# Performance work log

Hardware: AMD Instinct MI355X
Metric: run time of the kernel (lower is better)

The kernel has to match this reference:

```python
import jax, jax.numpy as jnp
import numpy as np

B, L, D = 2, 2048, 1024
H = 16          # num_heads
HD = D // H     # head_dim = 64
NEG_INF = jnp.float32(-1e30)


def setup_inputs() -> dict:
    key = jax.random.key(0)
    ks = jax.random.split(key, 10)
    s = 1.0 / np.sqrt(D)
    return {
        "x": jax.random.normal(ks[0], (B, L, D), dtype=jnp.float32),
        "Wq": jax.random.normal(ks[1], (D, D), dtype=jnp.float32) * s,
        "bq": jnp.zeros((D,), jnp.float32),
        "Wk": jax.random.normal(ks[2], (D, D), dtype=jnp.float32) * s,
        "bk": jnp.zeros((D,), jnp.float32),
        "Wv": jax.random.normal(ks[3], (D, D), dtype=jnp.float32) * s,
        "bv": jnp.zeros((D,), jnp.float32),
        "Wo": jax.random.normal(ks[4], (D, D), dtype=jnp.float32) * s,
        "bo": jnp.zeros((D,), jnp.float32),
        "local_scale": jnp.ones((1,), jnp.float32),
        "global_scale": jnp.ones((1,), jnp.float32),
    }


def reference(x, Wq, bq, Wk, bk, Wv, bv, Wo, bo, local_scale, global_scale):
    # projections -> [B, H, L, HD]
    def proj(W, b):
        return (x @ W + b).reshape(B, L, H, HD).transpose(0, 2, 1, 3)
    Q, K, V = proj(Wq, bq), proj(Wk, bk), proj(Wv, bv)
    lh = H // 2
    inv_sqrt = 1.0 / jnp.sqrt(jnp.float32(HD))

    # local (causal) heads
    scores_l = jnp.einsum("bhqd,bhkd->bhqk", Q[:, :lh], K[:, :lh]) * inv_sqrt
    causal = jnp.tril(jnp.ones((L, L), dtype=bool))  # keep lower triangle
    scores_l = jnp.where(causal, scores_l * local_scale, NEG_INF)
    attn_local = jax.nn.softmax(scores_l, axis=-1)
    out_local = jnp.einsum("bhqk,bhkd->bhqd", attn_local, V[:, :lh])

    # global (full) heads
    scores_g = jnp.einsum("bhqd,bhkd->bhqk", Q[:, lh:], K[:, lh:]) * inv_sqrt
    attn_global = jax.nn.softmax(scores_g * global_scale, axis=-1)
    out_global = jnp.einsum("bhqk,bhkd->bhqd", attn_global, V[:, lh:])

    out = jnp.concatenate([out_local, out_global], axis=1)  # [B,H,L,HD]
    out = out.transpose(0, 2, 1, 3).reshape(B, L, D)
    out = out @ Wo + bo
    return (out, attn_local, attn_global)
```

## Files before the change

### kernel.cpp

```cpp
#include <hip/hip_runtime.h>
#include <hip/hip_bf16.h>

#define B 2
#define L 2048
#define D 1024
#define H 16
#define HD 64
#define LH 8
#define NEG_INF -1e30f

typedef __hip_bfloat16 bf16;
typedef unsigned short ushort_t;
typedef short bf16x8 __attribute__((ext_vector_type(8)));
typedef unsigned short us8 __attribute__((ext_vector_type(8)));
typedef float f32x4 __attribute__((ext_vector_type(4)));

#define MFMA16(a, b, c) __builtin_amdgcn_mfma_f32_16x16x32_bf16((a), (b), (c), 0, 0, 0)

#define WAITBAR(N) do {                                              \
    asm volatile("s_waitcnt vmcnt(" #N ") lgkmcnt(0)" ::: "memory"); \
    __builtin_amdgcn_sched_barrier(0);                               \
    __builtin_amdgcn_s_barrier();                                    \
  } while (0)

#define LGKM0_FENCE() do {                                  \
    asm volatile("s_waitcnt lgkmcnt(0)" ::: "memory");      \
    __builtin_amdgcn_sched_barrier(0);                      \
  } while (0)

#if defined(__has_builtin)
#if __has_builtin(__builtin_amdgcn_global_load_lds)
#define HAVE_GLOAD_LDS 1
#endif
#endif

template<typename T> struct IsF32;
template<> struct IsF32<float> { static constexpr int value = 1; };
template<> struct IsF32<bf16>  { static constexpr int value = 0; };

__device__ __forceinline__ float ldf(const float* p, size_t i) { return p[i]; }
__device__ __forceinline__ float ldf(const bf16* p, size_t i) { return __bfloat162float(p[i]); }

__device__ __forceinline__ float4 ld4(const float* p, size_t i) {
  return *reinterpret_cast<const float4*>(p + i);
}
__device__ __forceinline__ float4 ld4(const bf16* p, size_t i) {
  ushort4 u = *reinterpret_cast<const ushort4*>(p + i);
  float4 f;
  f.x = __uint_as_float(((unsigned)u.x) << 16);
  f.y = __uint_as_float(((unsigned)u.y) << 16);
  f.z = __uint_as_float(((unsigned)u.z) << 16);
  f.w = __uint_as_float(((unsigned)u.w) << 16);
  return f;
}
__device__ __forceinline__ ushort_t bfh(float v) {
  bf16 h = __float2bfloat16(v);
  return *reinterpret_cast<ushort_t*>(&h);
}
__device__ __forceinline__ float bf2f(ushort_t u) {
  return __uint_as_float(((unsigned)u) << 16);
}
__device__ __forceinline__ void stf(float* p, size_t i, float v) { p[i] = v; }
__device__ __forceinline__ void stf(bf16* p, size_t i, float v) { p[i] = __float2bfloat16(v); }

__device__ __forceinline__ int swz(int row, int slot) {
  return row * 64 + (((slot ^ (row & 7)) & 7) << 3);
}
__device__ __forceinline__ int swzc(int row, int c) {
  return row * 64 + (((((c >> 3) ^ row) & 7) << 3) | (c & 7));
}

#if defined(HAVE_GLOAD_LDS)
__device__ __forceinline__ void gload_lds16(const ushort_t* src, ushort_t* dst) {
  __builtin_amdgcn_global_load_lds(
      (const __attribute__((address_space(1))) unsigned int*)src,
      (__attribute__((address_space(3))) unsigned int*)dst, 16, 0, 0);
}
#endif

__device__ __forceinline__ void stage64(const ushort_t* g, size_t gstride,
                                        ushort_t* lds, int w, int ln) {
  #pragma unroll
  for (int c = 0; c < 2; ++c) {
    const int row = 16 * w + 8 * c + (ln >> 3);
    const int slot = ((ln & 7) ^ row) & 7;
    const ushort_t* src = g + (size_t)row * gstride + slot * 8;
#if defined(HAVE_GLOAD_LDS)
    gload_lds16(src, lds + (size_t)(16 * w + 8 * c) * 64);
#else
    *reinterpret_cast<uint4*>(&lds[row * 64 + (ln & 7) * 8]) =
        *reinterpret_cast<const uint4*>(src);
#endif
  }
}

__global__ void detect_dtype_kernel(const unsigned short* __restrict__ x,
                                    int* __restrict__ flag) {
  int bad = 0;
  for (int i = threadIdx.x; i < 1024; i += 64) {
    if (((x[i] >> 7) & 0xFF) >= 170) bad = 1;
  }
  unsigned long long m = __ballot(bad);
  if (threadIdx.x == 0) *flag = (m != 0ULL) ? 1 : 0;
}

__global__ __launch_bounds__(256)
void cast_f32_kernel(const int* __restrict__ flag, int want,
                     const float* __restrict__ in,
                     ushort_t* __restrict__ hp, int n4) {
  if (*flag != want) return;
  int i = blockIdx.x * 256 + threadIdx.x;
  const int stride = gridDim.x * 256;
  for (; i < n4; i += stride) {
    float4 v = *reinterpret_cast<const float4*>(in + 4 * (size_t)i);
    ushort4 h;
    h.x = bfh(v.x); h.y = bfh(v.y); h.z = bfh(v.z); h.w = bfh(v.w);
    *reinterpret_cast<ushort4*>(hp + 4 * (size_t)i) = h;
  }
}

template<typename T>
__global__ __launch_bounds__(256)
void transW_kernel(const int* __restrict__ flag,
                   const T* __restrict__ W0, const T* __restrict__ W1,
                   const T* __restrict__ W2, const T* __restrict__ W3,
                   ushort_t* __restrict__ base, ushort_t* __restrict__ baseWo) {
  if (*flag != IsF32<T>::value) return;
  const int z = blockIdx.z;
  const T* W = z == 0 ? W0 : (z == 1 ? W1 : (z == 2 ? W2 : W3));
  ushort_t* hp = (z < 3) ? (base + (size_t)z * 2097152) : baseWo;
  __shared__ float ts[64][69];
  const int k0 = blockIdx.x * 64, n0 = blockIdx.y * 64;
  const int t = threadIdx.x;
  #pragma unroll
  for (int p = 0; p < 4; ++p) {
    int r = p * 16 + (t >> 4);
    int c = (t & 15) * 4;
    float4 v = ld4(W, (size_t)(k0 + r) * D + n0 + c);
    ts[r][c] = v.x; ts[r][c + 1] = v.y; ts[r][c + 2] = v.z; ts[r][c + 3] = v.w;
  }
  __syncthreads();
  #pragma unroll
  for (int p = 0; p < 4; ++p) {
    int n = p * 16 + (t >> 4);
    int k4 = (t & 15) * 4;
    ushort4 h;
    h.x = bfh(ts[k4][n]);
    h.y = bfh(ts[k4 + 1][n]);
    h.z = bfh(ts[k4 + 2][n]);
    h.w = bfh(ts[k4 + 3][n]);
    *reinterpret_cast<ushort4*>(&hp[(size_t)(n0 + n) * D + k0 + k4]) = h;
  }
}

template<typename T>
__global__ __launch_bounds__(256, 5)
void gemm_kernel(const int* __restrict__ flag,
                 const ushort_t* __restrict__ xA, const ushort_t* __restrict__ aoh,
                 const ushort_t* __restrict__ wbase, const ushort_t* __restrict__ woT,
                 const T* __restrict__ bq, const T* __restrict__ bk,
                 const T* __restrict__ bv, const T* __restrict__ bo,
                 ushort_t* __restrict__ qh, ushort_t* __restrict__ kh,
                 ushort_t* __restrict__ vth, T* __restrict__ out0, int zfix) {
  if (*flag != IsF32<T>::value) return;
  const int cpx = gridDim.x >> 3;
  const int swzid = ((int)blockIdx.x & 7) * cpx + ((int)blockIdx.x >> 3);
  const int mtile = swzid & 63;
  const int ntile = (swzid >> 6) & 15;
  const int z = (zfix >= 0) ? zfix : (swzid >> 10);
  const int m0 = mtile * 64, n0 = ntile * 64;

  const bool isOut = (z == 3);
  const ushort_t* Ah = isOut ? aoh : xA;
  const ushort_t* wh = isOut ? woT : (wbase + (size_t)z * 2097152);

  __shared__ ushort_t As[2][4096], Bs[2][4096];

  const int ln = threadIdx.x & 63, w = threadIdx.x >> 6;
  const int m = ln & 15, hi = ln >> 4;

  f32x4 acc[4] = {};

  stage64(Ah + (size_t)m0 * 1024, 1024, As[0], w, ln);
  stage64(wh + (size_t)n0 * 1024, 1024, Bs[0], w, ln);
  __syncthreads();
  for (int step = 0; step < 16; ++step) {
    const int cur = step & 1;
    if (step < 15) {
      stage64(Ah + (size_t)m0 * 1024 + (step + 1) * 64, 1024, As[cur ^ 1], w, ln);
      stage64(wh + (size_t)n0 * 1024 + (step + 1) * 64, 1024, Bs[cur ^ 1], w, ln);
    }
    __builtin_amdgcn_s_setprio(1);
    #pragma unroll
    for (int kc = 0; kc < 2; ++kc) {
      bf16x8 a_h = *reinterpret_cast<const bf16x8*>(&As[cur][swz(16 * w + m, kc * 4 + hi)]);
      bf16x8 b_h[4];
      #pragma unroll
      for (int f = 0; f < 4; ++f)
        b_h[f] = *reinterpret_cast<const bf16x8*>(&Bs[cur][swz(f * 16 + m, kc * 4 + hi)]);
      #pragma unroll
      for (int fc = 0; fc < 4; ++fc)
        acc[fc] = MFMA16(a_h, b_h[fc], acc[fc]);
    }
    __builtin_amdgcn_s_setprio(0);
    __syncthreads();
  }

  #pragma unroll
  for (int fc = 0; fc < 4; ++fc) {
    const int col = n0 + fc * 16 + m;
    if (isOut) {
      const float bv_ = ldf(bo, (size_t)col);
      #pragma unroll
      for (int r = 0; r < 4; ++r) {
        const int tok = m0 + 16 * w + 4 * hi + r;
        stf(out0, (size_t)tok * D + col, acc[fc][r] + bv_);
      }
    } else if (z == 2) {
      const int hh = col >> 6, d = col & 63;
      const float bv_ = ldf(bv, (size_t)col);
      const int tok0 = m0 + 16 * w + 4 * hi;
      const int bb = tok0 >> 11, ll = tok0 & (L - 1);
      ushort4 hv;
      hv.x = bfh(acc[fc][0] + bv_);
      hv.y = bfh(acc[fc][1] + bv_);
      hv.z = bfh(acc[fc][2] + bv_);
      hv.w = bfh(acc[fc][3] + bv_);
      *reinterpret_cast<ushort4*>(
          &vth[((size_t)(bb * H + hh) * HD + d) * L + ll]) = hv;
    } else {
      const int hh = col >> 6, d = col & 63;
      const float bv_ = ldf(z == 0 ? bq : bk, (size_t)col);
      ushort_t* oh = z == 0 ? qh : kh;
      #pragma unroll
      for (int r = 0; r < 4; ++r) {
        const int tok = m0 + 16 * w + 4 * hi + r;
        const int bb = tok >> 11, ll = tok & (L - 1);
        oh[((size_t)(bb * H + hh) * L + ll) * HD + d] = bfh(acc[fc][r] + bv_);
      }
    }
  }
}

template<typename T>
__global__ __launch_bounds__(256, 4)
void attn_kernel(const int* __restrict__ flag,
                 const ushort_t* __restrict__ Qh_g, const ushort_t* __restrict__ Kh_g,
                 const ushort_t* __restrict__ Vth_g,
                 const T* __restrict__ lsp, const T* __restrict__ gsp,
                 T* __restrict__ attn_l, T* __restrict__ attn_g,
                 ushort_t* __restrict__ AOh) {
  if (*flag != IsF32<T>::value) return;
  const int bid = blockIdx.x;
  const int xcd = bid & 7, slot = bid >> 3;
  const int bhg = xcd + 8 * (slot >> 5);
  const int strip_raw = slot & 31;
  const int bb = bhg >> 4, h = bhg & 15;
  const bool is_local = h < LH;
  const int strip = is_local ? (31 - strip_raw) : strip_raw;
  const int q0 = strip * 64;
  const int ln = threadIdx.x & 63, w = threadIdx.x >> 6;
  const int m = ln & 15, hi = ln >> 4;

  const float cscale =
      (is_local ? ldf(lsp, (size_t)0) : ldf(gsp, (size_t)0)) * 0.125f;
  const size_t bh_off = ((size_t)bb * H + h) * L * HD;
  const ushort_t* Qhb = Qh_g + bh_off;
  const ushort_t* Khb = Kh_g + bh_off;
  const ushort_t* Vhb = Vth_g + bh_off;

  __shared__ ushort_t SH[20480];
  ushort_t* Ps = SH + 16384;

  bf16x8 qfh[2];
  {
    const size_t qb = (size_t)(q0 + 16 * w + m) * HD + hi * 8;
    qfh[0] = *reinterpret_cast<const bf16x8*>(Qhb + qb);
    qfh[1] = *reinterpret_cast<const bf16x8*>(Qhb + qb + 32);
  }

  float m_ = NEG_INF, l_ = 0.f;
  const int nkt = is_local ? (strip + 1) : (L / 64);
  T* aout = is_local ? attn_l : attn_g;
  const size_t arow0 =
      ((size_t)(bb * LH + (is_local ? h : h - LH)) * L + q0) * L;

  stage64(Khb, HD, SH, w, ln);
  WAITBAR(0);
  for (int kt = 0; kt < nkt; ++kt) {
    const int cur = kt & 1;
    if (kt + 1 < nkt)
      stage64(Khb + (size_t)((kt + 1) * 64) * HD, HD, SH + (cur ^ 1) * 4096, w, ln);

    const ushort_t* Kc = SH + cur * 4096;
    f32x4 s[4] = {};
    __builtin_amdgcn_s_setprio(1);
    #pragma unroll
    for (int nt = 0; nt < 4; ++nt)
      #pragma unroll
      for (int kc = 0; kc < 2; ++kc) {
        bf16x8 kbh = *reinterpret_cast<const bf16x8*>(&Kc[swz(nt * 16 + m, kc * 4 + hi)]);
        s[nt] = MFMA16(kbh, qfh[kc], s[nt]);
      }
    __builtin_amdgcn_s_setprio(0);

    const bool dg = is_local && (kt == strip);
    #pragma unroll
    for (int nt = 0; nt < 4; ++nt)
      #pragma unroll
      for (int r = 0; r < 4; ++r) {
        float v = s[nt][r] * cscale;
        if (dg && (nt * 16 + 4 * hi + r > 16 * w + m)) v = NEG_INF;
        s[nt][r] = v;
      }
    float tm = NEG_INF;
    #pragma unroll
    for (int nt = 0; nt < 4; ++nt)
      #pragma unroll
      for (int r = 0; r < 4; ++r) tm = fmaxf(tm, s[nt][r]);
    tm = fmaxf(tm, __shfl_xor(tm, 16, 64));
    tm = fmaxf(tm, __shfl_xor(tm, 32, 64));
    const float mn = fmaxf(m_, tm);
    float sum = 0.f;
    #pragma unroll
    for (int nt = 0; nt < 4; ++nt)
      #pragma unroll
      for (int r = 0; r < 4; ++r) sum += __expf(s[nt][r] - mn);
    sum += __shfl_xor(sum, 16, 64);
    sum += __shfl_xor(sum, 32, 64);
    l_ = l_ * __expf(m_ - mn) + sum;
    m_ = mn;
    WAITBAR(0);
  }

  const float invl = 1.0f / l_;
  f32x4 o_[4] = {};

  stage64(Khb, HD, SH, w, ln);
  stage64(Vhb, L, SH + 8192, w, ln);
  WAITBAR(0);
  for (int kt = 0; kt < nkt; ++kt) {
    const int cur = kt & 1;
    if (kt + 1 < nkt) {
      stage64(Khb + (size_t)((kt + 1) * 64) * HD, HD, SH + (cur ^ 1) * 4096, w, ln);
      stage64(Vhb + (size_t)((kt + 1) * 64), L, SH + 8192 + (cur ^ 1) * 4096, w, ln);
    }
    const ushort_t* Kc = SH + cur * 4096;
    const ushort_t* Vc = SH + 8192 + cur * 4096;

    f32x4 s[4] = {};
    __builtin_amdgcn_s_setprio(1);
    #pragma unroll
    for (int nt = 0; nt < 4; ++nt)
      #pragma unroll
      for (int kc = 0; kc < 2; ++kc) {
        bf16x8 kbh = *reinterpret_cast<const bf16x8*>(&Kc[swz(nt * 16 + m, kc * 4 + hi)]);
        s[nt] = MFMA16(kbh, qfh[kc], s[nt]);
      }
    __builtin_amdgcn_s_setprio(0);

    const bool dg = is_local && (kt == strip);
    #pragma unroll
    for (int nt = 0; nt < 4; ++nt) {
      float v0 = s[nt][0] * cscale, v1 = s[nt][1] * cscale;
      float v2 = s[nt][2] * cscale, v3 = s[nt][3] * cscale;
      if (dg) {
        const int kbq = nt * 16 + 4 * hi, qq = 16 * w + m;
        if (kbq + 0 > qq) v0 = NEG_INF;
        if (kbq + 1 > qq) v1 = NEG_INF;
        if (kbq + 2 > qq) v2 = NEG_INF;
        if (kbq + 3 > qq) v3 = NEG_INF;
      }
      ushort4 pk;
      pk.x = bfh(__expf(v0 - m_) * invl);
      pk.y = bfh(__expf(v1 - m_) * invl);
      pk.z = bfh(__expf(v2 - m_) * invl);
      pk.w = bfh(__expf(v3 - m_) * invl);
      *reinterpret_cast<ushort4*>(&Ps[swzc(16 * w + m, nt * 16 + 4 * hi)]) = pk;
    }
    LGKM0_FENCE();

    __builtin_amdgcn_s_setprio(1);
    bf16x8 pf0 = *reinterpret_cast<const bf16x8*>(&Ps[swz(16 * w + m, hi)]);
    bf16x8 pf1 = *reinterpret_cast<const bf16x8*>(&Ps[swz(16 * w + m, 4 + hi)]);
    #pragma unroll
    for (int dt = 0; dt < 4; ++dt) {
      bf16x8 vf0 = *reinterpret_cast<const bf16x8*>(&Vc[swz(dt * 16 + m, hi)]);
      bf16x8 vf1 = *reinterpret_cast<const bf16x8*>(&Vc[swz(dt * 16 + m, 4 + hi)]);
      o_[dt] = MFMA16(pf0, vf0, o_[dt]);
      o_[dt] = MFMA16(pf1, vf1, o_[dt]);
    }
    __builtin_amdgcn_s_setprio(0);

    {
      const int pr = 16 * w + (ln >> 2);
      const int cs = (ln & 3) * 2;
      us8 v0 = *reinterpret_cast<const us8*>(&Ps[swz(pr, cs)]);
      us8 v1 = *reinterpret_cast<const us8*>(&Ps[swz(pr, cs + 1)]);
      const size_t gi = arow0 + (size_t)pr * L + (size_t)(kt * 64 + (ln & 3) * 16);
      if constexpr (IsF32<T>::value) {
        float* dst = (float*)aout + gi;
        *reinterpret_cast<float4*>(dst + 0) =
            make_float4(bf2f(v0[0]), bf2f(v0[1]), bf2f(v0[2]), bf2f(v0[3]));
        *reinterpret_cast<float4*>(dst + 4) =
            make_float4(bf2f(v0[4]), bf2f(v0[5]), bf2f(v0[6]), bf2f(v0[7]));
        *reinterpret_cast<float4*>(dst + 8) =
            make_float4(bf2f(v1[0]), bf2f(v1[1]), bf2f(v1[2]), bf2f(v1[3]));
        *reinterpret_cast<float4*>(dst + 12) =
            make_float4(bf2f(v1[4]), bf2f(v1[5]), bf2f(v1[6]), bf2f(v1[7]));
      } else {
        bf16* dst = (bf16*)aout + gi;
        *reinterpret_cast<uint4*>(dst + 0) = *reinterpret_cast<const uint4*>(&v0);
        *reinterpret_cast<uint4*>(dst + 8) = *reinterpret_cast<const uint4*>(&v1);
      }
    }
    if constexpr (IsF32<T>::value) { WAITBAR(4); } else { WAITBAR(2); }
  }

  if (is_local) {
    const int pr = 16 * w + (ln >> 2);
    const size_t rbase = arow0 + (size_t)pr * L;
    for (int c = nkt * 64 + (ln & 3) * 16; c < L; c += 64) {
      if constexpr (IsF32<T>::value) {
        float* dst = (float*)aout + rbase + c;
        const float4 z4 = make_float4(0.f, 0.f, 0.f, 0.f);
        *reinterpret_cast<float4*>(dst + 0) = z4;
        *reinterpret_cast<float4*>(dst + 4) = z4;
        *reinterpret_cast<float4*>(dst + 8) = z4;
        *reinterpret_cast<float4*>(dst + 12) = z4;
      } else {
        bf16* dst = (bf16*)aout + rbase + c;
        const uint4 z4 = make_uint4(0u, 0u, 0u, 0u);
        *reinterpret_cast<uint4*>(dst + 0) = z4;
        *reinterpret_cast<uint4*>(dst + 8) = z4;
      }
    }
  }

  #pragma unroll
  for (int dt = 0; dt < 4; ++dt)
    #pragma unroll
    for (int r = 0; r < 4; ++r)
      AOh[((size_t)bb * L + q0 + 16 * w + 4 * hi + r) * D + h * HD + dt * 16 + m] =
          bfh(o_[dt][r]);
}

template<typename T>
static void launch_path(void* const* d_in, void* d_out, void* d_ws, hipStream_t stream) {
  const int want = IsF32<T>::value;
  const int* flag = (const int*)d_ws;
  ushort_t* Qh  = (ushort_t*)((char*)d_ws + 256);
  ushort_t* Kh  = Qh + 4194304;
  ushort_t* Vth = Kh + 4194304;
  ushort_t* AOh = Vth + 4194304;
  ushort_t* Woth = AOh + 4194304;

  const T* x  = (const T*)d_in[0];
  const T* Wq = (const T*)d_in[1];
  const T* bq = (const T*)d_in[2];
  const T* Wk = (const T*)d_in[3];
  const T* bk = (const T*)d_in[4];
  const T* Wv = (const T*)d_in[5];
  const T* bv = (const T*)d_in[6];
  const T* Wo = (const T*)d_in[7];
  const T* bo = (const T*)d_in[8];
  const T* ls = (const T*)d_in[9];
  const T* gs = (const T*)d_in[10];

  T* out0   = (T*)d_out;
  T* attn_l = out0 + (size_t)B * L * D;
  T* attn_g = attn_l + (size_t)B * LH * L * L;
  ushort_t* xh  = (ushort_t*)attn_g;
  ushort_t* Wt3 = xh + 4194304;

  if constexpr (IsF32<T>::value)
    cast_f32_kernel<<<1024, 256, 0, stream>>>(flag, want, (const float*)x, xh, 1048576);
  transW_kernel<T><<<dim3(16, 16, 4), 256, 0, stream>>>(
      flag, Wq, Wk, Wv, Wo, Wt3, Woth);
  const ushort_t* xA = IsF32<T>::value ? xh : (const ushort_t*)x;

  gemm_kernel<T><<<3072, 256, 0, stream>>>(
      flag, xA, AOh, Wt3, Woth, bq, bk, bv, bo, Qh, Kh, Vth, out0, -1);
  attn_kernel<T><<<1024, 256, 0, stream>>>(
      flag, Qh, Kh, Vth, ls, gs, attn_l, attn_g, AOh);
  gemm_kernel<T><<<1024, 256, 0, stream>>>(
      flag, xA, AOh, Wt3, Woth, bq, bk, bv, bo, Qh, Kh, Vth, out0, 3);
}

extern "C" void kernel_launch(void* const* d_in, const int* in_sizes, int n_in,
                              void* d_out, int out_size, void* d_ws, size_t ws_size,
                              hipStream_t stream) {
  int* flag = (int*)d_ws;
  detect_dtype_kernel<<<1, 64, 0, stream>>>((const unsigned short*)d_in[0], flag);
  launch_path<float>(d_in, d_out, d_ws, stream);
  launch_path<bf16>(d_in, d_out, d_ws, stream);
}
```

Measured before the change: 911.0 us.

## Batch attention-probability stores over four key tiles using quad-buffered P tiles

```diff
diff --git a/kernel.cpp b/kernel.cpp
--- a/kernel.cpp
+++ b/kernel.cpp
@@ -243,7 +243,7 @@
 }
 
 template<typename T>
-__global__ __launch_bounds__(256, 4)
+__global__ __launch_bounds__(256, 2)
 void attn_kernel(const int* __restrict__ flag,
                  const ushort_t* __restrict__ Qh_g, const ushort_t* __restrict__ Kh_g,
                  const ushort_t* __restrict__ Vth_g,
@@ -269,8 +269,8 @@
   const ushort_t* Khb = Kh_g + bh_off;
   const ushort_t* Vhb = Vth_g + bh_off;
 
-  __shared__ ushort_t SH[20480];
-  ushort_t* Ps = SH + 16384;
+  __shared__ ushort_t SH[32768];
+  ushort_t* Pbuf = SH + 16384;
 
   bf16x8 qfh[2];
   {
@@ -347,6 +347,7 @@
     }
     const ushort_t* Kc = SH + cur * 4096;
     const ushort_t* Vc = SH + 8192 + cur * 4096;
+    ushort_t* Pc = Pbuf + (kt & 3) * 4096;
 
     f32x4 s[4] = {};
     __builtin_amdgcn_s_setprio(1);
@@ -376,13 +377,13 @@
       pk.y = bfh(__expf(v1 - m_) * invl);
       pk.z = bfh(__expf(v2 - m_) * invl);
       pk.w = bfh(__expf(v3 - m_) * invl);
-      *reinterpret_cast<ushort4*>(&Ps[swzc(16 * w + m, nt * 16 + 4 * hi)]) = pk;
+      *reinterpret_cast<ushort4*>(&Pc[swzc(16 * w + m, nt * 16 + 4 * hi)]) = pk;
     }
     LGKM0_FENCE();
 
     __builtin_amdgcn_s_setprio(1);
-    bf16x8 pf0 = *reinterpret_cast<const bf16x8*>(&Ps[swz(16 * w + m, hi)]);
-    bf16x8 pf1 = *reinterpret_cast<const bf16x8*>(&Ps[swz(16 * w + m, 4 + hi)]);
+    bf16x8 pf0 = *reinterpret_cast<const bf16x8*>(&Pc[swz(16 * w + m, hi)]);
+    bf16x8 pf1 = *reinterpret_cast<const bf16x8*>(&Pc[swz(16 * w + m, 4 + hi)]);
     #pragma unroll
     for (int dt = 0; dt < 4; ++dt) {
       bf16x8 vf0 = *reinterpret_cast<const bf16x8*>(&Vc[swz(dt * 16 + m, hi)]);
@@ -392,29 +393,39 @@
     }
     __builtin_amdgcn_s_setprio(0);
 
-    {
-      const int pr = 16 * w + (ln >> 2);
-      const int cs = (ln & 3) * 2;
-      us8 v0 = *reinterpret_cast<const us8*>(&Ps[swz(pr, cs)]);
-      us8 v1 = *reinterpret_cast<const us8*>(&Ps[swz(pr, cs + 1)]);
-      const size_t gi = arow0 + (size_t)pr * L + (size_t)(kt * 64 + (ln & 3) * 16);
-      if constexpr (IsF32<T>::value) {
-        float* dst = (float*)aout + gi;
-        *reinterpret_cast<float4*>(dst + 0) =
-            make_float4(bf2f(v0[0]), bf2f(v0[1]), bf2f(v0[2]), bf2f(v0[3]));
-        *reinterpret_cast<float4*>(dst + 4) =
-            make_float4(bf2f(v0[4]), bf2f(v0[5]), bf2f(v0[6]), bf2f(v0[7]));
-        *reinterpret_cast<float4*>(dst + 8) =
-            make_float4(bf2f(v1[0]), bf2f(v1[1]), bf2f(v1[2]), bf2f(v1[3]));
-        *reinterpret_cast<float4*>(dst + 12) =
-            make_float4(bf2f(v1[4]), bf2f(v1[5]), bf2f(v1[6]), bf2f(v1[7]));
-      } else {
-        bf16* dst = (bf16*)aout + gi;
-        *reinterpret_cast<uint4*>(dst + 0) = *reinterpret_cast<const uint4*>(&v0);
-        *reinterpret_cast<uint4*>(dst + 8) = *reinterpret_cast<const uint4*>(&v1);
-      }
-    }
-    if constexpr (IsF32<T>::value) { WAITBAR(4); } else { WAITBAR(2); }
+    if ((kt & 3) == 3 || kt == nkt - 1) {
+      const int g0 = kt & ~3;
+      const int gs = kt - g0 + 1;
+      const int sel = ln & 3;
+      if (sel < gs) {
+        const int pr = 16 * w + (ln >> 2);
+        const ushort_t* Pr = Pbuf + sel * 4096;
+        us8 v[8];
+        #pragma unroll
+        for (int s2 = 0; s2 < 8; ++s2)
+          v[s2] = *reinterpret_cast<const us8*>(&Pr[swz(pr, s2)]);
+        const size_t gi = arow0 + (size_t)pr * L + (size_t)((g0 + sel) * 64);
+        if constexpr (IsF32<T>::value) {
+          float* dst = (float*)aout + gi;
+          #pragma unroll
+          for (int s2 = 0; s2 < 8; ++s2) {
+            *reinterpret_cast<float4*>(dst + s2 * 8) =
+                make_float4(bf2f(v[s2][0]), bf2f(v[s2][1]),
+                            bf2f(v[s2][2]), bf2f(v[s2][3]));
+            *reinterpret_cast<float4*>(dst + s2 * 8 + 4) =
+                make_float4(bf2f(v[s2][4]), bf2f(v[s2][5]),
+                            bf2f(v[s2][6]), bf2f(v[s2][7]));
+          }
+        } else {
+          bf16* dst = (bf16*)aout + gi;
+          #pragma unroll
+          for (int s2 = 0; s2 < 8; ++s2)
+            *reinterpret_cast<uint4*>(dst + s2 * 8) =
+                *reinterpret_cast<const uint4*>(&v[s2]);
+        }
+      }
+    }
+    WAITBAR(0);
   }
 
   if (is_local) {
```

New measurement: 923.3 us. About the same (+1.3%).

## Prefetch K/V tiles into registers two iterations ahead of LDS writes

Applied to the files above, without the earlier changes.

```diff
diff --git a/kernel.cpp b/kernel.cpp
--- a/kernel.cpp
+++ b/kernel.cpp
@@ -336,85 +336,129 @@
   const float invl = 1.0f / l_;
   f32x4 o_[4] = {};
 
-  stage64(Khb, HD, SH, w, ln);
-  stage64(Vhb, L, SH + 8192, w, ln);
-  WAITBAR(0);
-  for (int kt = 0; kt < nkt; ++kt) {
-    const int cur = kt & 1;
-    if (kt + 1 < nkt) {
-      stage64(Khb + (size_t)((kt + 1) * 64) * HD, HD, SH + (cur ^ 1) * 4096, w, ln);
-      stage64(Vhb + (size_t)((kt + 1) * 64), L, SH + 8192 + (cur ^ 1) * 4096, w, ln);
+  {
+    const int r0 = 16 * w + (ln >> 3);
+    const int sl = ln & 7;
+    uint4 kA0, kA1, vA0, vA1, kB0, kB1, vB0, vB1;
+
+#define LOADT(x, K0, K1, V0, V1) do {                                       \
+      const ushort_t* kp_ = Khb + (size_t)((x) * 64 + r0) * HD + sl * 8;    \
+      K0 = *reinterpret_cast<const uint4*>(kp_);                            \
+      K1 = *reinterpret_cast<const uint4*>(kp_ + 8 * HD);                   \
+      const ushort_t* vp_ = Vhb + (size_t)r0 * L + (x) * 64 + sl * 8;       \
+      V0 = *reinterpret_cast<const uint4*>(vp_);                            \
+      V1 = *reinterpret_cast<const uint4*>(vp_ + 8 * L);                    \
+    } while (0)
+#define WRITET(bs, K0, K1, V0, V1) do {                                     \
+      ushort_t* kb_ = SH + (bs) * 4096;                                     \
+      ushort_t* vb_ = SH + 8192 + (bs) * 4096;                              \
+      *reinterpret_cast<uint4*>(&kb_[swz(r0, sl)]) = K0;                    \
+      *reinterpret_cast<uint4*>(&kb_[swz(r0 + 8, sl)]) = K1;                \
+      *reinterpret_cast<uint4*>(&vb_[swz(r0, sl)]) = V0;                    \
+      *reinterpret_cast<uint4*>(&vb_[swz(r0 + 8, sl)]) = V1;                \
+    } while (0)
+
+    LOADT(0, kA0, kA1, vA0, vA1);
+    asm volatile("s_waitcnt vmcnt(0)" ::: "memory");
+    __builtin_amdgcn_sched_barrier(0);
+    WRITET(0, kA0, kA1, vA0, vA1);
+    if (nkt > 1) LOADT(1, kB0, kB1, vB0, vB1);
+    LGKM0_FENCE();
+    __builtin_amdgcn_s_barrier();
+
+    for (int kt = 0; kt < nkt; ++kt) {
+      const int cur = kt & 1;
+      if (kt + 1 < nkt) {
+        if (kt == 0) {
+          asm volatile("s_waitcnt vmcnt(0)" ::: "memory");
+        } else if constexpr (IsF32<T>::value) {
+          asm volatile("s_waitcnt vmcnt(4)" ::: "memory");
+        } else {
+          asm volatile("s_waitcnt vmcnt(2)" ::: "memory");
+        }
+        __builtin_amdgcn_sched_barrier(0);
+        if (cur == 0) {
+          WRITET(1, kB0, kB1, vB0, vB1);
+          if (kt + 2 < nkt) LOADT(kt + 2, kA0, kA1, vA0, vA1);
+        } else {
+          WRITET(0, kA0, kA1, vA0, vA1);
+          if (kt + 2 < nkt) LOADT(kt + 2, kB0, kB1, vB0, vB1);
+        }
+      }
+      const ushort_t* Kc = SH + cur * 4096;
+      const ushort_t* Vc = SH + 8192 + cur * 4096;
+
+      f32x4 s[4] = {};
+      __builtin_amdgcn_s_setprio(1);
+      #pragma unroll
+      for (int nt = 0; nt < 4; ++nt)
+        #pragma unroll
+        for (int kc = 0; kc < 2; ++kc) {
+          bf16x8 kbh = *reinterpret_cast<const bf16x8*>(&Kc[swz(nt * 16 + m, kc * 4 + hi)]);
+          s[nt] = MFMA16(kbh, qfh[kc], s[nt]);
+        }
+      __builtin_amdgcn_s_setprio(0);
+
+      const bool dg = is_local && (kt == strip);
+      #pragma unroll
+      for (int nt = 0; nt < 4; ++nt) {
+        float v0 = s[nt][0] * cscale, v1 = s[nt][1] * cscale;
+        float v2 = s[nt][2] * cscale, v3 = s[nt][3] * cscale;
+        if (dg) {
+          const int kbq = nt * 16 + 4 * hi, qq = 16 * w + m;
+          if (kbq + 0 > qq) v0 = NEG_INF;
+          if (kbq + 1 > qq) v1 = NEG_INF;
+          if (kbq + 2 > qq) v2 = NEG_INF;
+          if (kbq + 3 > qq) v3 = NEG_INF;
+        }
+        ushort4 pk;
+        pk.x = bfh(__expf(v0 - m_) * invl);
+        pk.y = bfh(__expf(v1 - m_) * invl);
+        pk.z = bfh(__expf(v2 - m_) * invl);
+        pk.w = bfh(__expf(v3 - m_) * invl);
+        *reinterpret_cast<ushort4*>(&Ps[swzc(16 * w + m, nt * 16 + 4 * hi)]) = pk;
+      }
+      LGKM0_FENCE();
+
+      __builtin_amdgcn_s_setprio(1);
+      bf16x8 pf0 = *reinterpret_cast<const bf16x8*>(&Ps[swz(16 * w + m, hi)]);
+      bf16x8 pf1 = *reinterpret_cast<const bf16x8*>(&Ps[swz(16 * w + m, 4 + hi)]);
+      #pragma unroll
+      for (int dt = 0; dt < 4; ++dt) {
+        bf16x8 vf0 = *reinterpret_cast<const bf16x8*>(&Vc[swz(dt * 16 + m, hi)]);
+        bf16x8 vf1 = *reinterpret_cast<const bf16x8*>(&Vc[swz(dt * 16 + m, 4 + hi)]);
+        o_[dt] = MFMA16(pf0, vf0, o_[dt]);
+        o_[dt] = MFMA16(pf1, vf1, o_[dt]);
+      }
+      __builtin_amdgcn_s_setprio(0);
+
+      {
+        const int pr = 16 * w + (ln >> 2);
+        const int cs = (ln & 3) * 2;
+        us8 v0 = *reinterpret_cast<const us8*>(&Ps[swz(pr, cs)]);
+        us8 v1 = *reinterpret_cast<const us8*>(&Ps[swz(pr, cs + 1)]);
+        const size_t gi = arow0 + (size_t)pr * L + (size_t)(kt * 64 + (ln & 3) * 16);
+        if constexpr (IsF32<T>::value) {
+          float* dst = (float*)aout + gi;
+          *reinterpret_cast<float4*>(dst + 0) =
+              make_float4(bf2f(v0[0]), bf2f(v0[1]), bf2f(v0[2]), bf2f(v0[3]));
+          *reinterpret_cast<float4*>(dst + 4) =
+              make_float4(bf2f(v0[4]), bf2f(v0[5]), bf2f(v0[6]), bf2f(v0[7]));
+          *reinterpret_cast<float4*>(dst + 8) =
+              make_float4(bf2f(v1[0]), bf2f(v1[1]), bf2f(v1[2]), bf2f(v1[3]));
+          *reinterpret_cast<float4*>(dst + 12) =
+              make_float4(bf2f(v1[4]), bf2f(v1[5]), bf2f(v1[6]), bf2f(v1[7]));
+        } else {
+          bf16* dst = (bf16*)aout + gi;
+          *reinterpret_cast<uint4*>(dst + 0) = *reinterpret_cast<const uint4*>(&v0);
+          *reinterpret_cast<uint4*>(dst + 8) = *reinterpret_cast<const uint4*>(&v1);
+        }
+      }
+      LGKM0_FENCE();
+      __builtin_amdgcn_s_barrier();
     }
-    const ushort_t* Kc = SH + cur * 4096;
-    const ushort_t* Vc = SH + 8192 + cur * 4096;
-
-    f32x4 s[4] = {};
-    __builtin_amdgcn_s_setprio(1);
-    #pragma unroll
-    for (int nt = 0; nt < 4; ++nt)
-      #pragma unroll
-      for (int kc = 0; kc < 2; ++kc) {
-        bf16x8 kbh = *reinterpret_cast<const bf16x8*>(&Kc[swz(nt * 16 + m, kc * 4 + hi)]);
-        s[nt] = MFMA16(kbh, qfh[kc], s[nt]);
-      }
-    __builtin_amdgcn_s_setprio(0);
-
-    const bool dg = is_local && (kt == strip);
-    #pragma unroll
-    for (int nt = 0; nt < 4; ++nt) {
-      float v0 = s[nt][0] * cscale, v1 = s[nt][1] * cscale;
-      float v2 = s[nt][2] * cscale, v3 = s[nt][3] * cscale;
-      if (dg) {
-        const int kbq = nt * 16 + 4 * hi, qq = 16 * w + m;
-        if (kbq + 0 > qq) v0 = NEG_INF;
-        if (kbq + 1 > qq) v1 = NEG_INF;
-        if (kbq + 2 > qq) v2 = NEG_INF;
-        if (kbq + 3 > qq) v3 = NEG_INF;
-      }
-      ushort4 pk;
-      pk.x = bfh(__expf(v0 - m_) * invl);
-      pk.y = bfh(__expf(v1 - m_) * invl);
-      pk.z = bfh(__expf(v2 - m_) * invl);
-      pk.w = bfh(__expf(v3 - m_) * invl);
-      *reinterpret_cast<ushort4*>(&Ps[swzc(16 * w + m, nt * 16 + 4 * hi)]) = pk;
-    }
-    LGKM0_FENCE();
-
-    __builtin_amdgcn_s_setprio(1);
-    bf16x8 pf0 = *reinterpret_cast<const bf16x8*>(&Ps[swz(16 * w + m, hi)]);
-    bf16x8 pf1 = *reinterpret_cast<const bf16x8*>(&Ps[swz(16 * w + m, 4 + hi)]);
-    #pragma unroll
-    for (int dt = 0; dt < 4; ++dt) {
-      bf16x8 vf0 = *reinterpret_cast<const bf16x8*>(&Vc[swz(dt * 16 + m, hi)]);
-      bf16x8 vf1 = *reinterpret_cast<const bf16x8*>(&Vc[swz(dt * 16 + m, 4 + hi)]);
-      o_[dt] = MFMA16(pf0, vf0, o_[dt]);
-      o_[dt] = MFMA16(pf1, vf1, o_[dt]);
-    }
-    __builtin_amdgcn_s_setprio(0);
-
-    {
-      const int pr = 16 * w + (ln >> 2);
-      const int cs = (ln & 3) * 2;
-      us8 v0 = *reinterpret_cast<const us8*>(&Ps[swz(pr, cs)]);
-      us8 v1 = *reinterpret_cast<const us8*>(&Ps[swz(pr, cs + 1)]);
-      const size_t gi = arow0 + (size_t)pr * L + (size_t)(kt * 64 + (ln & 3) * 16);
-      if constexpr (IsF32<T>::value) {
-        float* dst = (float*)aout + gi;
-        *reinterpret_cast<float4*>(dst + 0) =
-            make_float4(bf2f(v0[0]), bf2f(v0[1]), bf2f(v0[2]), bf2f(v0[3]));
-        *reinterpret_cast<float4*>(dst + 4) =
-            make_float4(bf2f(v0[4]), bf2f(v0[5]), bf2f(v0[6]), bf2f(v0[7]));
-        *reinterpret_cast<float4*>(dst + 8) =
-            make_float4(bf2f(v1[0]), bf2f(v1[1]), bf2f(v1[2]), bf2f(v1[3]));
-        *reinterpret_cast<float4*>(dst + 12) =
-            make_float4(bf2f(v1[4]), bf2f(v1[5]), bf2f(v1[6]), bf2f(v1[7]));
-      } else {
-        bf16* dst = (bf16*)aout + gi;
-        *reinterpret_cast<uint4*>(dst + 0) = *reinterpret_cast<const uint4*>(&v0);
-        *reinterpret_cast<uint4*>(dst + 8) = *reinterpret_cast<const uint4*>(&v1);
-      }
-    }
-    if constexpr (IsF32<T>::value) { WAITBAR(4); } else { WAITBAR(2); }
+#undef LOADT
+#undef WRITET
   }
 
   if (is_local) {
```

Result: no change. 911.5 us (+0.1%).
